# Kernel optimization log

Hardware: AMD Instinct MI355X
Metric: run time of the kernel (lower is better)

The kernel has to match this reference:

```python
import jax, jax.numpy as jnp
import numpy as np

EPS = 1e-5
HD = 16          # hidden_dim
OC = 256         # out_chs
NH = 8           # num_heads (groups of qkv conv)
DV = OC // (2 * HD)  # per-head value dim = 8


def conv_bn_silu(x, w, gamma, beta, mean, var, stride=1, pad=1, groups=1):
    # Conv2d(bias=False) + BatchNorm2d(eval) + SiLU, NCHW/OIHW
    y = jax.lax.conv_general_dilated(
        x, w, (stride, stride), [(pad, pad), (pad, pad)],
        dimension_numbers=('NCHW', 'OIHW', 'NCHW'),
        feature_group_count=groups)
    inv = gamma * jax.lax.rsqrt(var + EPS)
    y = y * inv[None, :, None, None] + (beta - mean * inv)[None, :, None, None]
    return y * jax.nn.sigmoid(y)


def _bn_params(key, c):
    k1, k2, k3, k4 = jax.random.split(key, 4)
    g = 1.0 + 0.1 * jax.random.normal(k1, (c,), jnp.float32)
    b = 0.1 * jax.random.normal(k2, (c,), jnp.float32)
    m = 0.1 * jax.random.normal(k3, (c,), jnp.float32)
    v = jax.random.uniform(k4, (c,), jnp.float32, 0.5, 1.5)
    return g, b, m, v


def setup_inputs() -> dict:
    key = jax.random.key(0)
    ks = jax.random.split(key, 8)
    B, C, H, W = 16, 256, 80, 80
    qkv_out = HD * 2 + OC // 2  # 160
    d = {}
    d['x'] = jax.random.normal(ks[0], (B, C, H, W), jnp.float32)
    # qkv_conv: grouped 3x3, groups=NH -> in per group = C//NH
    d['qkv_w'] = jax.random.normal(ks[1], (qkv_out, C // NH, 3, 3), jnp.float32) * 0.05
    d['qkv_g'], d['qkv_b'], d['qkv_m'], d['qkv_v'] = _bn_params(ks[2], qkv_out)
    # hidden_conv: dense 3x3
    d['hid_w'] = jax.random.normal(ks[3], (OC, C, 3, 3), jnp.float32) * 0.02
    d['hid_g'], d['hid_b'], d['hid_m'], d['hid_v'] = _bn_params(ks[4], OC)
    # out_conv: 1x1 on (OC//2*3) channels
    d['out_w'] = jax.random.normal(ks[5], (OC, OC // 2 * 3, 1, 1), jnp.float32) * 0.05
    d['out_g'], d['out_b'], d['out_m'], d['out_v'] = _bn_params(ks[6], OC)
    return d


def reference(x, qkv_w, qkv_g, qkv_b, qkv_m, qkv_v,
              hid_w, hid_g, hid_b, hid_m, hid_v,
              out_w, out_g, out_b, out_m, out_v):
    B, C, H, W = x.shape
    N = H * W
    qkv = conv_bn_silu(x, qkv_w, qkv_g, qkv_b, qkv_m, qkv_v, stride=1, pad=1, groups=NH)
    q = qkv[:, :HD]               # (B, HD, H, W)
    k = qkv[:, HD:2 * HD]
    v = qkv[:, 2 * HD:]           # (B, OC//2, H, W)
    # permute to (B, N, HD) / (B, N, HD, DV), channel-major reshape matches torch .view
    q = q.transpose(0, 2, 3, 1).reshape(B, N, HD)
    k = k.transpose(0, 2, 3, 1).reshape(B, N, HD)
    v = v.transpose(0, 2, 3, 1).reshape(B, N, HD, DV)
    # per-pixel tiny attention: attn[b,n,i,j] = softmax_j(q_i * k_j)
    attn = jax.nn.softmax(q[..., :, None] * k[..., None, :], axis=-1)  # (B,N,HD,HD)
    y = jnp.einsum('bnij,bnjd->bnid', attn, v)                          # (B,N,HD,DV)
    # torch: permute(0,2,3,1).view(B, OC//2, H, W)
    y = y.transpose(0, 2, 3, 1).reshape(B, OC // 2, H, W)
    h = conv_bn_silu(x, hid_w, hid_g, hid_b, hid_m, hid_v, stride=1, pad=1)
    y = jnp.concatenate([y, h], axis=1)  # (B, OC//2*3, H, W)
    return conv_bn_silu(y, out_w, out_g, out_b, out_m, out_v, stride=1, pad=0)
```

## Files before the change

kernel.cpp:

```cpp
#include <hip/hip_runtime.h>
#include <stdint.h>

typedef unsigned short u16;
typedef unsigned int u32;
typedef __attribute__((ext_vector_type(4))) float f32x4;
typedef __attribute__((ext_vector_type(8))) __bf16 bf16x8;

#define EPS_BN 1e-5f

__device__ __forceinline__ u16 f2bf(float f) {
  u32 u = __builtin_bit_cast(u32, f);
  u32 r = (u + 0x7fffu + ((u >> 16) & 1u)) >> 16;
  return (u16)r;
}

__device__ __forceinline__ float silu_f(float v) {
  return v / (1.0f + __expf(-v));
}

__device__ __forceinline__ void gll16(const void* g, void* l) {
  __builtin_amdgcn_global_load_lds(
      (__attribute__((address_space(1))) void*)(void*)g,
      (__attribute__((address_space(3))) void*)l, 16, 0, 0);
}

__global__ __launch_bounds__(256) void prep(
    const float* __restrict__ qkv_w, const float* __restrict__ qg,
    const float* __restrict__ qb, const float* __restrict__ qm,
    const float* __restrict__ qv,
    const float* __restrict__ hid_w, const float* __restrict__ hg,
    const float* __restrict__ hb, const float* __restrict__ hm,
    const float* __restrict__ hv,
    const float* __restrict__ out_w, const float* __restrict__ og,
    const float* __restrict__ ob, const float* __restrict__ om,
    const float* __restrict__ ov,
    u16* __restrict__ wtb, u16* __restrict__ w2b, u16* __restrict__ wqp,
    float* __restrict__ bnq_s, float* __restrict__ bnq_b,
    float* __restrict__ bnh_s, float* __restrict__ bnh_b,
    float* __restrict__ bn2s, float* __restrict__ bn2b,
    float* __restrict__ zpg)
{
  const int gid = blockIdx.x * 256 + threadIdx.x;
  if (gid < 256 * 2304) {
    int j = gid / 2304, k = gid - j * 2304;
    int tap = k >> 8, c = k & 255;
    wtb[gid] = f2bf(hid_w[(j * 256 + c) * 9 + tap]);
  }
  if (gid < 73728) {
    int g = gid / 9216;
    int r = gid - g * 9216;
    int j = r / 288, k = r - j * 288;
    int tap = k >> 5, cg = k & 31;
    float v = 0.f;
    if (j < 20) v = qkv_w[((g * 20 + j) * 32 + cg) * 9 + tap];
    wqp[gid] = f2bf(v);
  }
  if (gid < 98304) w2b[gid] = f2bf(out_w[gid]);
  if (gid < 160) {
    float iv = qg[gid] * rsqrtf(qv[gid] + EPS_BN);
    bnq_s[gid] = iv; bnq_b[gid] = qb[gid] - qm[gid] * iv;
  }
  if (gid < 256) {
    float iv = hg[gid] * rsqrtf(hv[gid] + EPS_BN);
    bnh_s[gid] = iv; bnh_b[gid] = hb[gid] - hm[gid] * iv;
    float iv2 = og[gid] * rsqrtf(ov[gid] + EPS_BN);
    bn2s[gid] = iv2; bn2b[gid] = ob[gid] - om[gid] * iv2;
  }
  if (gid < 64) zpg[gid] = 0.f;
}

__global__ __launch_bounds__(256) void nchw2nhwc(
    const float* __restrict__ x, u16* __restrict__ xn)
{
  __shared__ u16 T[80 * 66];
  const int t = threadIdx.x;
  const int ct = blockIdx.x;
  const int h  = blockIdx.y;
  const int b  = blockIdx.z;
  const float* src = x + ((size_t)b * 256 + ct * 64) * 6400 + h * 80;
  for (int it = 0; it < 5; ++it) {
    int idx = it * 256 + t;
    int cl = idx / 20, w4 = idx - cl * 20;
    float4 v = *(const float4*)(src + (size_t)cl * 6400 + w4 * 4);
    T[(w4 * 4 + 0) * 66 + cl] = f2bf(v.x);
    T[(w4 * 4 + 1) * 66 + cl] = f2bf(v.y);
    T[(w4 * 4 + 2) * 66 + cl] = f2bf(v.z);
    T[(w4 * 4 + 3) * 66 + cl] = f2bf(v.w);
  }
  __syncthreads();
  u16* dst = xn + ((size_t)(b * 80 + h) * 80) * 256 + ct * 64;
  for (int it = 0; it < 5; ++it) {
    int idx = it * 256 + t;
    int wl = idx >> 4;
    int cl = (idx & 15) * 4;
    ushort4 v4;
    v4.x = T[wl * 66 + cl + 0];
    v4.y = T[wl * 66 + cl + 1];
    v4.z = T[wl * 66 + cl + 2];
    v4.w = T[wl * 66 + cl + 3];
    *(ushort4*)(dst + (size_t)wl * 256 + cl) = v4;
  }
}

__global__ __launch_bounds__(256, 2) void gemm_main(
    const u16* __restrict__ xn, const u16* __restrict__ wt,
    const float* __restrict__ bns, const float* __restrict__ bnb,
    const float* __restrict__ zpg, u16* __restrict__ ycat)
{
  __shared__ __attribute__((aligned(16))) u16 Al[128 * 64];
  __shared__ __attribute__((aligned(16))) u16 Bl[128 * 64];
  const int t = threadIdx.x;
  const int wave = t >> 6, lane = t & 63;
  const int wr = wave >> 1, wc = wave & 1;
  const int orig = blockIdx.y * 2 + blockIdx.x;
  const int wg = (orig & 7) * 200 + (orig >> 3);
  const int jtile = (wg / 800) * 128;
  const int ptile = (wg % 800) * 128;

  const int srcc = (((lane & 7) ^ ((lane >> 3) & 7)) * 8);
  int pb[4], hh[4], wwv[4], bofB[4];
#pragma unroll
  for (int c = 0; c < 4; ++c) {
    int m = wave * 32 + c * 8 + (lane >> 3);
    int p = ptile + m;
    pb[c] = p;
    int hw = p % 6400;
    hh[c] = hw / 80;
    wwv[c] = hw - (hw / 80) * 80;
    bofB[c] = (jtile + m) * 2304 + srcc;
  }
  u16* AlW = Al + wave * 2048;
  u16* BlW = Bl + wave * 2048;

  f32x4 acc[4][4];
#pragma unroll
  for (int m = 0; m < 4; ++m)
#pragma unroll
    for (int n = 0; n < 4; ++n) {
      f32x4 z = {0.f, 0.f, 0.f, 0.f};
      acc[m][n] = z;
    }

  for (int ks = 0; ks < 36; ++ks) {
    const int k0 = ks * 64;
    const int tap = k0 >> 8;
    const int c0 = k0 & 255;
    const int dh = tap / 3 - 1, dw = tap - (tap / 3) * 3 - 1;
    __syncthreads();
#pragma unroll
    for (int c = 0; c < 4; ++c) {
      int h2 = hh[c] + dh, w2 = wwv[c] + dw;
      bool ok = ((unsigned)h2 < 80u) & ((unsigned)w2 < 80u);
      const u16* src = ok
          ? (xn + ((size_t)(pb[c] + dh * 80 + dw) * 256 + c0 + srcc))
          : (const u16*)zpg;
      gll16(src, AlW + c * 512);
    }
#pragma unroll
    for (int c = 0; c < 4; ++c)
      gll16(wt + (size_t)(bofB[c] + k0), BlW + c * 512);
    __syncthreads();
#pragma unroll
    for (int kk = 0; kk < 2; ++kk) {
      const int q = kk * 4 + (lane >> 4);
      const int c16 = lane & 15;
      bf16x8 av[4], bv[4];
#pragma unroll
      for (int m = 0; m < 4; ++m) {
        int r = wr * 64 + m * 16 + c16;
        av[m] = *(const bf16x8*)(Al + r * 64 + (q ^ (r & 7)) * 8);
      }
#pragma unroll
      for (int n = 0; n < 4; ++n) {
        int r = wc * 64 + n * 16 + c16;
        bv[n] = *(const bf16x8*)(Bl + r * 64 + (q ^ (r & 7)) * 8);
      }
#pragma unroll
      for (int m = 0; m < 4; ++m)
#pragma unroll
        for (int n = 0; n < 4; ++n)
          acc[m][n] = __builtin_amdgcn_mfma_f32_16x16x32_bf16(
              av[m], bv[n], acc[m][n], 0, 0, 0);
    }
  }

  const int c16 = lane & 15, rg = lane >> 4;
#pragma unroll
  for (int n = 0; n < 4; ++n) {
    int j = jtile + wc * 64 + n * 16 + c16;
    float sc = bns[j], bi = bnb[j];
#pragma unroll
    for (int m = 0; m < 4; ++m) {
      int p0 = ptile + wr * 64 + m * 16 + rg * 4;
#pragma unroll
      for (int r = 0; r < 4; ++r) {
        float v = silu_f(acc[m][n][r] * sc + bi);
        ycat[(size_t)(p0 + r) * 384 + 128 + j] = f2bf(v);
      }
    }
  }
}

__global__ __launch_bounds__(256, 2) void qkv_gemm(
    const u16* __restrict__ xn, const u16* __restrict__ wqp,
    const float* __restrict__ bnq_s, const float* __restrict__ bnq_b,
    const float* __restrict__ zpg, float* __restrict__ qkvb)
{
  __shared__ __attribute__((aligned(16))) u16 Al[128 * 64];
  const int t = threadIdx.x;
  const int wave = t >> 6, lane = t & 63;
  const int orig = blockIdx.x;
  const int wg = (orig & 7) * 100 + (orig >> 3);
  const int ptile = wg * 128;

  const int srcc = (((lane & 7) ^ ((lane >> 3) & 7)) * 8);
  int pb[4], hh[4], wwv[4];
#pragma unroll
  for (int c = 0; c < 4; ++c) {
    int m = wave * 32 + c * 8 + (lane >> 3);
    int p = ptile + m;
    pb[c] = p;
    int hw = p % 6400;
    hh[c] = hw / 80;
    wwv[c] = hw - (hw / 80) * 80;
  }
  u16* AlW = Al + wave * 2048;

  const int q = lane >> 4, c16 = lane & 15;
  f32x4 acc[2][16];
#pragma unroll
  for (int m = 0; m < 2; ++m)
#pragma unroll
    for (int f = 0; f < 16; ++f) {
      f32x4 z = {0.f, 0.f, 0.f, 0.f};
      acc[m][f] = z;
    }

  for (int tap = 0; tap < 9; ++tap) {
    const int dh = tap / 3 - 1, dw = tap - (tap / 3) * 3 - 1;
    const int dp = dh * 80 + dw;
#pragma unroll
    for (int cc = 0; cc < 4; ++cc) {
      const int c0 = cc * 64;
      __syncthreads();
#pragma unroll
      for (int c = 0; c < 4; ++c) {
        int h2 = hh[c] + dh, w2 = wwv[c] + dw;
        bool ok = ((unsigned)h2 < 80u) & ((unsigned)w2 < 80u);
        const u16* src = ok
            ? (xn + ((size_t)(pb[c] + dp) * 256 + c0 + srcc))
            : (const u16*)zpg;
        gll16(src, AlW + c * 512);
      }
      bf16x8 bv[2][2];
#pragma unroll
      for (int h = 0; h < 2; ++h)
#pragma unroll
        for (int nf = 0; nf < 2; ++nf) {
          int row = (2 * cc + h) * 32 + nf * 16 + c16;
          bv[h][nf] = *(const bf16x8*)(wqp + (size_t)row * 288 + tap * 32 + q * 8);
        }
      __syncthreads();
      bf16x8 av[2][2];
#pragma unroll
      for (int m = 0; m < 2; ++m) {
        int r = wave * 32 + m * 16 + c16;
#pragma unroll
        for (int h = 0; h < 2; ++h) {
          int q8 = h * 4 + q;
          av[m][h] = *(const bf16x8*)(Al + r * 64 + (q8 ^ (r & 7)) * 8);
        }
      }
#pragma unroll
      for (int h = 0; h < 2; ++h)
#pragma unroll
        for (int m = 0; m < 2; ++m)
#pragma unroll
          for (int nf = 0; nf < 2; ++nf)
            acc[m][(2 * cc + h) * 2 + nf] = __builtin_amdgcn_mfma_f32_16x16x32_bf16(
                av[m][h], bv[h][nf], acc[m][(2 * cc + h) * 2 + nf], 0, 0, 0);
    }
  }

#pragma unroll
  for (int f = 0; f < 16; ++f) {
    int jj = (f & 1) * 16 + c16;
    if (jj >= 20) continue;
    int oc = (f >> 1) * 20 + jj;
    float sc = bnq_s[oc], bi = bnq_b[oc];
#pragma unroll
    for (int m = 0; m < 2; ++m) {
      int p0 = ptile + wave * 32 + m * 16 + q * 4;
#pragma unroll
      for (int r = 0; r < 4; ++r)
        qkvb[(size_t)(p0 + r) * 160 + oc] = silu_f(acc[m][f][r] * sc + bi);
    }
  }
}

__global__ __launch_bounds__(256) void attn_k(
    const float* __restrict__ qkvb, u16* __restrict__ ycat)
{
  __shared__ float qs[16 * 168];
  const int t = threadIdx.x;
  const size_t p0 = (size_t)blockIdx.x * 16;
  const float* src = qkvb + p0 * 160;
  for (int idx = t; idx < 2560; idx += 256) {
    int r = idx / 160;
    qs[r * 168 + (idx - r * 160)] = src[idx];
  }
  __syncthreads();
  const int px = t >> 4, i = t & 15;
  const float* row = qs + px * 168;
  const float qi = row[i];
  float s[16];
  float mx = -3.4e38f;
#pragma unroll
  for (int j = 0; j < 16; ++j) { s[j] = qi * row[16 + j]; mx = fmaxf(mx, s[j]); }
  float sum = 0.f;
#pragma unroll
  for (int j = 0; j < 16; ++j) { s[j] = __expf(s[j] - mx); sum += s[j]; }
  const float inv = 1.0f / sum;
  float y[8];
#pragma unroll
  for (int d = 0; d < 8; ++d) y[d] = 0.f;
#pragma unroll
  for (int j = 0; j < 16; ++j) {
    const float a = s[j];
    const float* vr = row + 32 + j * 8;
#pragma unroll
    for (int d = 0; d < 8; ++d) y[d] += a * vr[d];
  }
  union { u16 u[8]; uint4 v4; } pk;
#pragma unroll
  for (int d = 0; d < 8; ++d) pk.u[d] = f2bf(y[d] * inv);
  *(uint4*)(ycat + (p0 + px) * 384 + i * 8) = pk.v4;
}

__global__ __launch_bounds__(256, 2) void gemm_out(
    const u16* __restrict__ w2, const u16* __restrict__ ycat,
    const float* __restrict__ bns, const float* __restrict__ bnb,
    float* __restrict__ out)
{
  __shared__ __attribute__((aligned(16))) u16 Al[128 * 64];
  __shared__ __attribute__((aligned(16))) u16 Bl[128 * 64];
  const int t = threadIdx.x;
  const int wave = t >> 6, lane = t & 63;
  const int wr = wave >> 1, wc = wave & 1;
  const int orig = blockIdx.y * 2 + blockIdx.x;
  const int wg = (orig & 7) * 200 + (orig >> 3);
  const int octile = (wg / 800) * 128;
  const int ptile = (wg % 800) * 128;

  const int srcc = (((lane & 7) ^ ((lane >> 3) & 7)) * 8);
  int bofA[4], bofB[4];
#pragma unroll
  for (int c = 0; c < 4; ++c) {
    int m = wave * 32 + c * 8 + (lane >> 3);
    bofA[c] = (octile + m) * 384 + srcc;
    bofB[c] = (ptile + m) * 384 + srcc;
  }
  u16* AlW = Al + wave * 2048;
  u16* BlW = Bl + wave * 2048;

  f32x4 acc[4][4];
#pragma unroll
  for (int m = 0; m < 4; ++m)
#pragma unroll
    for (int n = 0; n < 4; ++n) {
      f32x4 z = {0.f, 0.f, 0.f, 0.f};
      acc[m][n] = z;
    }

  for (int ks = 0; ks < 6; ++ks) {
    const int k0 = ks * 64;
    __syncthreads();
#pragma unroll
    for (int c = 0; c < 4; ++c) gll16(w2 + (size_t)(bofA[c] + k0), AlW + c * 512);
#pragma unroll
    for (int c = 0; c < 4; ++c) gll16(ycat + (size_t)(bofB[c] + k0), BlW + c * 512);
    __syncthreads();
#pragma unroll
    for (int kk = 0; kk < 2; ++kk) {
      const int q = kk * 4 + (lane >> 4);
      const int c16 = lane & 15;
      bf16x8 av[4], bv[4];
#pragma unroll
      for (int m = 0; m < 4; ++m) {
        int r = wr * 64 + m * 16 + c16;
        av[m] = *(const bf16x8*)(Al + r * 64 + (q ^ (r & 7)) * 8);
      }
#pragma unroll
      for (int n = 0; n < 4; ++n) {
        int r = wc * 64 + n * 16 + c16;
        bv[n] = *(const bf16x8*)(Bl + r * 64 + (q ^ (r & 7)) * 8);
      }
#pragma unroll
      for (int m = 0; m < 4; ++m)
#pragma unroll
        for (int n = 0; n < 4; ++n)
          acc[m][n] = __builtin_amdgcn_mfma_f32_16x16x32_bf16(
              av[m], bv[n], acc[m][n], 0, 0, 0);
    }
  }

  const int c16 = lane & 15, rg = lane >> 4;
  const int b = ptile / 6400;
  const int hwb = ptile - b * 6400;
#pragma unroll
  for (int m = 0; m < 4; ++m) {
    int oc0 = octile + wr * 64 + m * 16 + rg * 4;
#pragma unroll
    for (int n = 0; n < 4; ++n) {
      int hw = hwb + wc * 64 + n * 16 + c16;
#pragma unroll
      for (int r = 0; r < 4; ++r) {
        int oc = oc0 + r;
        float v = silu_f(acc[m][n][r] * bns[oc] + bnb[oc]);
        out[((size_t)b * 256 + oc) * 6400 + hw] = v;
      }
    }
  }
}

extern "C" void kernel_launch(void* const* d_in, const int* in_sizes, int n_in,
                              void* d_out, int out_size, void* d_ws, size_t ws_size,
                              hipStream_t stream) {
  (void)in_sizes; (void)n_in; (void)out_size; (void)ws_size;
  const float* x    = (const float*)d_in[0];
  const float* qkvw = (const float*)d_in[1];
  const float* qg   = (const float*)d_in[2];
  const float* qb   = (const float*)d_in[3];
  const float* qm   = (const float*)d_in[4];
  const float* qv   = (const float*)d_in[5];
  const float* hw_  = (const float*)d_in[6];
  const float* hg   = (const float*)d_in[7];
  const float* hb   = (const float*)d_in[8];
  const float* hm   = (const float*)d_in[9];
  const float* hv   = (const float*)d_in[10];
  const float* ow   = (const float*)d_in[11];
  const float* og   = (const float*)d_in[12];
  const float* ob   = (const float*)d_in[13];
  const float* om   = (const float*)d_in[14];
  const float* ov   = (const float*)d_in[15];

  char* ws = (char*)d_ws;
  float* zpg   = (float*)(ws + 0);
  float* bnq_s = (float*)(ws + 256);
  float* bnq_b = (float*)(ws + 1280);
  float* bnh_s = (float*)(ws + 2304);
  float* bnh_b = (float*)(ws + 3328);
  float* bn2s  = (float*)(ws + 4352);
  float* bn2b  = (float*)(ws + 5376);
  u16*   wtb   = (u16*)(ws + 6400);
  u16*   w2b   = (u16*)(ws + 1186048);
  u16*   wqp   = (u16*)(ws + 1382656);
  u16*   xn    = (u16*)(ws + 1536000);
  float* qkvb  = (float*)(ws + 53964800);
  u16*   ycat  = (u16*)(ws + 119500800);
  float* out   = (float*)d_out;

  prep<<<dim3(2304), dim3(256), 0, stream>>>(
      qkvw, qg, qb, qm, qv, hw_, hg, hb, hm, hv, ow, og, ob, om, ov,
      wtb, w2b, wqp, bnq_s, bnq_b, bnh_s, bnh_b, bn2s, bn2b, zpg);
  nchw2nhwc<<<dim3(4, 80, 16), dim3(256), 0, stream>>>(x, xn);
  gemm_main<<<dim3(2, 800), dim3(256), 0, stream>>>(
      xn, wtb, bnh_s, bnh_b, zpg, ycat);
  qkv_gemm<<<dim3(800), dim3(256), 0, stream>>>(
      xn, wqp, bnq_s, bnq_b, zpg, qkvb);
  attn_k<<<dim3(6400), dim3(256), 0, stream>>>(qkvb, ycat);
  gemm_out<<<dim3(2, 800), dim3(256), 0, stream>>>(
      w2b, ycat, bn2s, bn2b, out);
}
```

Baseline: 355.1 us.

## Double-buffer qkv_gemm LDS staging and prefetch next chunk's loads

Splits the qkv_gemm LDS tile into two buffers and issues the global-to-LDS loads and weight loads for the next (tap, channel-chunk) step before computing the current one. It relies on s_waitcnt vmcnt instead of block-wide __syncthreads, because each wave only reads the LDS rows it staged itself. The aim is to overlap global memory latency with MFMA work and remove barrier stalls. In exchange it doubles LDS use and adds register pressure for the second set of weight fragments, and it depends on a hand-written vmcnt count being correct.

```diff
diff --git a/kernel.cpp b/kernel.cpp
--- a/kernel.cpp
+++ b/kernel.cpp
@@ -206,7 +206,7 @@
     const float* __restrict__ bnq_s, const float* __restrict__ bnq_b,
     const float* __restrict__ zpg, float* __restrict__ qkvb)
 {
-  __shared__ __attribute__((aligned(16))) u16 Al[128 * 64];
+  __shared__ __attribute__((aligned(16))) u16 Al[2][128 * 64];
   const int t = threadIdx.x;
   const int wave = t >> 6, lane = t & 63;
   const int orig = blockIdx.x;
@@ -224,9 +224,38 @@
     hh[c] = hw / 80;
     wwv[c] = hw - (hw / 80) * 80;
   }
-  u16* AlW = Al + wave * 2048;
+  u16* AlW0 = Al[0] + wave * 2048;
+  u16* AlW1 = Al[1] + wave * 2048;
 
   const int q = lane >> 4, c16 = lane & 15;
+
+  auto STAGE = [&](int tap, int cc, u16* dst) {
+    if (tap > 8) tap = 8;
+    const int dh = tap / 3 - 1, dw = tap - (tap / 3) * 3 - 1;
+    const int dp = dh * 80 + dw;
+    const int c0 = cc * 64;
+#pragma unroll
+    for (int c = 0; c < 4; ++c) {
+      int h2 = hh[c] + dh, w2 = wwv[c] + dw;
+      bool ok = ((unsigned)h2 < 80u) & ((unsigned)w2 < 80u);
+      const u16* src = ok
+          ? (xn + ((size_t)(pb[c] + dp) * 256 + c0 + srcc))
+          : (const u16*)zpg;
+      gll16(src, dst + c * 512);
+    }
+  };
+  auto BQ = [&](int tap, int cc, bf16x8* bv) {
+    if (tap > 8) tap = 8;
+#pragma unroll
+    for (int h = 0; h < 2; ++h)
+#pragma unroll
+      for (int nf = 0; nf < 2; ++nf) {
+        int row = (2 * cc + h) * 32 + nf * 16 + c16;
+        bv[h * 2 + nf] =
+            *(const bf16x8*)(wqp + (size_t)row * 288 + tap * 32 + q * 8);
+      }
+  };
+
   f32x4 acc[2][16];
 #pragma unroll
   for (int m = 0; m < 2; ++m)
@@ -236,39 +265,29 @@
       acc[m][f] = z;
     }
 
+  bf16x8 bqA[4], bqB[4];
+  BQ(0, 0, bqA);
+  STAGE(0, 0, AlW0);
+
   for (int tap = 0; tap < 9; ++tap) {
-    const int dh = tap / 3 - 1, dw = tap - (tap / 3) * 3 - 1;
-    const int dp = dh * 80 + dw;
 #pragma unroll
     for (int cc = 0; cc < 4; ++cc) {
-      const int c0 = cc * 64;
-      __syncthreads();
-#pragma unroll
-      for (int c = 0; c < 4; ++c) {
-        int h2 = hh[c] + dh, w2 = wwv[c] + dw;
-        bool ok = ((unsigned)h2 < 80u) & ((unsigned)w2 < 80u);
-        const u16* src = ok
-            ? (xn + ((size_t)(pb[c] + dp) * 256 + c0 + srcc))
-            : (const u16*)zpg;
-        gll16(src, AlW + c * 512);
-      }
-      bf16x8 bv[2][2];
-#pragma unroll
-      for (int h = 0; h < 2; ++h)
-#pragma unroll
-        for (int nf = 0; nf < 2; ++nf) {
-          int row = (2 * cc + h) * 32 + nf * 16 + c16;
-          bv[h][nf] = *(const bf16x8*)(wqp + (size_t)row * 288 + tap * 32 + q * 8);
-        }
-      __syncthreads();
+      const int ntap = (cc == 3) ? tap + 1 : tap;
+      const int ncc = (cc + 1) & 3;
+      if ((cc & 1) == 0) { BQ(ntap, ncc, bqB); STAGE(ntap, ncc, AlW1); }
+      else               { BQ(ntap, ncc, bqA); STAGE(ntap, ncc, AlW0); }
+      asm volatile("s_waitcnt vmcnt(8)" ::: "memory");
+      __builtin_amdgcn_sched_barrier(0);
+      const u16* AW = ((cc & 1) == 0) ? AlW0 : AlW1;
+      const bf16x8* bq = ((cc & 1) == 0) ? bqA : bqB;
       bf16x8 av[2][2];
 #pragma unroll
       for (int m = 0; m < 2; ++m) {
-        int r = wave * 32 + m * 16 + c16;
+        int rl = m * 16 + c16;
 #pragma unroll
         for (int h = 0; h < 2; ++h) {
           int q8 = h * 4 + q;
-          av[m][h] = *(const bf16x8*)(Al + r * 64 + (q8 ^ (r & 7)) * 8);
+          av[m][h] = *(const bf16x8*)(AW + rl * 64 + ((q8 ^ (rl & 7)) * 8));
         }
       }
 #pragma unroll
@@ -278,7 +297,7 @@
 #pragma unroll
           for (int nf = 0; nf < 2; ++nf)
             acc[m][(2 * cc + h) * 2 + nf] = __builtin_amdgcn_mfma_f32_16x16x32_bf16(
-                av[m][h], bv[h][nf], acc[m][(2 * cc + h) * 2 + nf], 0, 0, 0);
+                av[m][h], bq[h * 2 + nf], acc[m][(2 * cc + h) * 2 + nf], 0, 0, 0);
     }
   }
 
```

Result: faster. 346.8 us (-2.3%).
